# Kernel tuning notes

Measured on AMD Instinct MI355X. Metric: run time of the kernel, lower is better.

Reference implementation:

```python
import jax, jax.numpy as jnp
import numpy as np

D_MODEL = 1024
NUM_HEADS = 16
HEAD_DIM = D_MODEL // NUM_HEADS
LN_EPS = 1e-5


def setup_inputs() -> dict:
    key = jax.random.key(0)
    ks = jax.random.split(key, 10)
    B, S, D = 4, 2048, D_MODEL
    scale = 1.0 / np.sqrt(D)
    inp = {
        'x': jax.random.normal(ks[0], (B, S, D), dtype=jnp.float32),
        'attention_mask': jnp.ones((B, S), dtype=jnp.float32),
        'Wq': jax.random.normal(ks[1], (D, D), dtype=jnp.float32) * scale,
        'bq': jnp.zeros((D,), dtype=jnp.float32),
        'Wk': jax.random.normal(ks[2], (D, D), dtype=jnp.float32) * scale,
        'bk': jnp.zeros((D,), dtype=jnp.float32),
        'Wv': jax.random.normal(ks[3], (D, D), dtype=jnp.float32) * scale,
        'bv': jnp.zeros((D,), dtype=jnp.float32),
        'Wo': jax.random.normal(ks[4], (D, D), dtype=jnp.float32) * scale,
        'bo': jnp.zeros((D,), dtype=jnp.float32),
        'ln_gamma': jnp.ones((D,), dtype=jnp.float32),
        'ln_beta': jnp.zeros((D,), dtype=jnp.float32),
    }
    return inp


def reference(x, attention_mask, Wq, bq, Wk, bk, Wv, bv, Wo, bo, ln_gamma, ln_beta):
    B, S, D = x.shape
    H, Hd = NUM_HEADS, HEAD_DIM
    identity = x
    # LayerNorm (eps matches torch default 1e-5)
    mu = jnp.mean(x, axis=-1, keepdims=True)
    var = jnp.mean(jnp.square(x - mu), axis=-1, keepdims=True)
    xn = (x - mu) / jnp.sqrt(var + LN_EPS) * ln_gamma + ln_beta
    # projections (torch Linear: x @ W.T + b); weights here stored as [out,in]-compatible square
    q = (xn @ Wq.T + bq).reshape(B, S, H, Hd).transpose(0, 2, 1, 3)  # [B,H,S,Hd]
    k = (xn @ Wk.T + bk).reshape(B, S, H, Hd).transpose(0, 2, 1, 3)
    v = (xn @ Wv.T + bv).reshape(B, S, H, Hd).transpose(0, 2, 1, 3)
    scores = jnp.einsum('bhqd,bhkd->bhqk', q, k) / jnp.sqrt(jnp.float32(Hd))
    # padding mask: [B,S] -> additive [B,1,1,S]
    add_mask = (1.0 - attention_mask)[:, None, None, :] * -10000.0
    scores = scores + add_mask
    # causal mask (strict upper triangle -> -inf)
    causal = jnp.triu(jnp.ones((S, S), dtype=bool), k=1)
    scores = jnp.where(causal[None, None, :, :], -jnp.inf, scores)
    attn = jax.nn.softmax(scores, axis=-1)
    out = jnp.einsum('bhqk,bhkd->bhqd', attn, v)  # [B,H,S,Hd]
    out = out.transpose(0, 2, 1, 3).reshape(B, S, D)
    out = out @ Wo.T + bo
    return identity + out
```

## Files before the change

kernel.cpp:

```cpp
#include <hip/hip_runtime.h>

#define D 1024
#define NH 16
#define HD 64
#define SEQ 2048
#define BATCH 4
#define LN_EPS 1e-5f
#define LOG2E 1.44269504088896f

typedef __attribute__((ext_vector_type(8))) __bf16 bf16x8;
typedef __attribute__((ext_vector_type(4))) float f32x4;

__device__ __forceinline__ ushort f2bf(float f) {
    union { float f; uint u; } c; c.f = f;
    uint u = c.u + 0x7fffu + ((c.u >> 16) & 1u);
    return (ushort)(u >> 16);
}

__device__ __forceinline__ void gl_lds16(const ushort* g, ushort* lds) {
    __builtin_amdgcn_global_load_lds(
        (const __attribute__((address_space(1))) void*)g,
        (__attribute__((address_space(3))) void*)lds, 16, 0, 0);
}

__device__ __forceinline__ float exp2_raw(float v) {
    float e;
    asm("v_exp_f32 %0, %1" : "=v"(e) : "v"(v));
    return e;
}

__global__ __launch_bounds__(256) void cvt4(const float* __restrict__ w0,
    const float* __restrict__ w1, const float* __restrict__ w2,
    const float* __restrict__ w3, ushort* __restrict__ out, int n)
{
    int sel = blockIdx.y;
    const float* in = sel == 0 ? w0 : (sel == 1 ? w1 : (sel == 2 ? w2 : w3));
    int i = (blockIdx.x * 256 + threadIdx.x) * 4;
    if (i < n) {
        float4 v = *(const float4*)(in + i);
        ushort4 o;
        o.x = f2bf(v.x); o.y = f2bf(v.y); o.z = f2bf(v.z); o.w = f2bf(v.w);
        *(ushort4*)(out + (size_t)sel * n + i) = o;
    }
}

__global__ __launch_bounds__(256) void ln_kernel(const float* __restrict__ x,
    const float* __restrict__ gamma, const float* __restrict__ beta,
    ushort* __restrict__ xn)
{
    int row = blockIdx.x;
    int tid = threadIdx.x;
    float4 v = ((const float4*)(x + (size_t)row * D))[tid];
    float s = v.x + v.y + v.z + v.w;
#pragma unroll
    for (int off = 32; off > 0; off >>= 1) s += __shfl_down(s, off, 64);
    __shared__ float red1[4], red2[4];
    int wid = tid >> 6, lane = tid & 63;
    if (lane == 0) red1[wid] = s;
    __syncthreads();
    float mean = (red1[0] + red1[1] + red1[2] + red1[3]) * (1.0f / D);
    float dx = v.x - mean, dy = v.y - mean, dz = v.z - mean, dw = v.w - mean;
    float ss = dx * dx + dy * dy + dz * dz + dw * dw;
#pragma unroll
    for (int off = 32; off > 0; off >>= 1) ss += __shfl_down(ss, off, 64);
    if (lane == 0) red2[wid] = ss;
    __syncthreads();
    float var = (red2[0] + red2[1] + red2[2] + red2[3]) * (1.0f / D);
    float rstd = rsqrtf(var + LN_EPS);
    float4 g = ((const float4*)gamma)[tid];
    float4 b = ((const float4*)beta)[tid];
    ushort4 o;
    o.x = f2bf(dx * rstd * g.x + b.x);
    o.y = f2bf(dy * rstd * g.y + b.y);
    o.z = f2bf(dz * rstd * g.z + b.z);
    o.w = f2bf(dw * rstd * g.w + b.w);
    ((ushort4*)(xn + (size_t)row * D))[tid] = o;
}

#define BM 128
#define BKK 64

__global__ __launch_bounds__(256) void gemm_qkv(
    const ushort* __restrict__ A,
    const ushort* __restrict__ W,
    const float* __restrict__ bq, const float* __restrict__ bk,
    const float* __restrict__ bv,
    ushort* __restrict__ Cq, ushort* __restrict__ Ck,
    ushort* __restrict__ CvT,
    int M, int K)
{
    __shared__ ushort As[2][BM * BKK];
    __shared__ ushort Ws[2][BM * BKK];
    const int tid = threadIdx.x;
    const int lane = tid & 63;
    const int wave = tid >> 6;
    const int wr = wave >> 1, wc = wave & 1;
    const int m0 = blockIdx.y * BM;
    const int n0g = blockIdx.x * BM;
    const int region = n0g >> 10;
    const int n0l = n0g & 1023;
    const float* bias = region == 0 ? bq : (region == 1 ? bk : bv);
    const int fr = lane & 15, quad = lane >> 4;
    const int r8 = lane >> 3, c8 = lane & 7;
    const int gc8 = c8 ^ r8;
    const int swf = fr & 7;

    const ushort* gA = A + (size_t)(m0 + wave * 32 + r8) * K + gc8 * 8;
    const ushort* gW = W + (size_t)(n0g + wave * 32 + r8) * K + gc8 * 8;
    const int ldso = (wave * 32) * BKK;

    f32x4 acc[4][4] = {};

#pragma unroll
    for (int t = 0; t < 4; ++t) {
        gl_lds16(gA + (size_t)t * 8 * K, &As[0][ldso + t * 8 * BKK]);
        gl_lds16(gW + (size_t)t * 8 * K, &Ws[0][ldso + t * 8 * BKK]);
    }
    __syncthreads();

    for (int k0 = 0; k0 < K; k0 += BKK) {
        const int cur = (k0 >> 6) & 1;
        if (k0 + BKK < K) {
            const int nxt = cur ^ 1;
#pragma unroll
            for (int t = 0; t < 4; ++t) {
                gl_lds16(gA + (size_t)t * 8 * K + k0 + BKK, &As[nxt][ldso + t * 8 * BKK]);
                gl_lds16(gW + (size_t)t * 8 * K + k0 + BKK, &Ws[nxt][ldso + t * 8 * BKK]);
            }
        }
#pragma unroll
        for (int kh = 0; kh < 2; ++kh) {
            bf16x8 af[4], bf[4];
            const int co = ((kh * 4 + quad) ^ swf) * 8;
#pragma unroll
            for (int i = 0; i < 4; ++i) {
                af[i] = *(const bf16x8*)&As[cur][(wr * 64 + i * 16 + fr) * BKK + co];
                bf[i] = *(const bf16x8*)&Ws[cur][(wc * 64 + i * 16 + fr) * BKK + co];
            }
#pragma unroll
            for (int i = 0; i < 4; ++i)
#pragma unroll
                for (int j = 0; j < 4; ++j)
                    acc[i][j] = __builtin_amdgcn_mfma_f32_16x16x32_bf16(af[i], bf[j], acc[i][j], 0, 0, 0);
        }
        __syncthreads();
    }

#pragma unroll
    for (int j = 0; j < 4; ++j) {
        int col = n0l + wc * 64 + j * 16 + fr;
        float bvl = bias[col];
#pragma unroll
        for (int i = 0; i < 4; ++i) {
#pragma unroll
            for (int r = 0; r < 4; ++r) {
                int row = m0 + wr * 64 + i * 16 + quad * 4 + r;
                ushort hv = f2bf(acc[i][j][r] + bvl);
                if (region == 0) {
                    Cq[(size_t)row * 1024 + col] = hv;
                } else if (region == 1) {
                    Ck[(size_t)row * 1024 + col] = hv;
                } else {
                    int bb = row >> 11, s = row & 2047;
                    int hh = col >> 6, d = col & 63;
                    CvT[(((size_t)bb * NH + hh) * HD + d) * SEQ + s] = hv;
                }
            }
        }
    }
}

__global__ __launch_bounds__(256) void gemm_out(
    const ushort* __restrict__ A, const ushort* __restrict__ W,
    const float* __restrict__ bias, const float* __restrict__ resid,
    float* __restrict__ Cf, int M, int N, int K)
{
    __shared__ ushort As[2][BM * BKK];
    __shared__ ushort Ws[2][BM * BKK];
    const int tid = threadIdx.x;
    const int lane = tid & 63;
    const int wave = tid >> 6;
    const int wr = wave >> 1, wc = wave & 1;
    const int m0 = blockIdx.y * BM, n0 = blockIdx.x * BM;
    const int fr = lane & 15, quad = lane >> 4;
    const int r8 = lane >> 3, c8 = lane & 7;
    const int gc8 = c8 ^ r8;
    const int swf = fr & 7;

    const ushort* gA = A + (size_t)(m0 + wave * 32 + r8) * K + gc8 * 8;
    const ushort* gW = W + (size_t)(n0 + wave * 32 + r8) * K + gc8 * 8;
    const int ldso = (wave * 32) * BKK;

    f32x4 acc[4][4] = {};

#pragma unroll
    for (int t = 0; t < 4; ++t) {
        gl_lds16(gA + (size_t)t * 8 * K, &As[0][ldso + t * 8 * BKK]);
        gl_lds16(gW + (size_t)t * 8 * K, &Ws[0][ldso + t * 8 * BKK]);
    }
    __syncthreads();

    for (int k0 = 0; k0 < K; k0 += BKK) {
        const int cur = (k0 >> 6) & 1;
        if (k0 + BKK < K) {
            const int nxt = cur ^ 1;
#pragma unroll
            for (int t = 0; t < 4; ++t) {
                gl_lds16(gA + (size_t)t * 8 * K + k0 + BKK, &As[nxt][ldso + t * 8 * BKK]);
                gl_lds16(gW + (size_t)t * 8 * K + k0 + BKK, &Ws[nxt][ldso + t * 8 * BKK]);
            }
        }
#pragma unroll
        for (int kh = 0; kh < 2; ++kh) {
            bf16x8 af[4], bf[4];
            const int co = ((kh * 4 + quad) ^ swf) * 8;
#pragma unroll
            for (int i = 0; i < 4; ++i) {
                af[i] = *(const bf16x8*)&As[cur][(wr * 64 + i * 16 + fr) * BKK + co];
                bf[i] = *(const bf16x8*)&Ws[cur][(wc * 64 + i * 16 + fr) * BKK + co];
            }
#pragma unroll
            for (int i = 0; i < 4; ++i)
#pragma unroll
                for (int j = 0; j < 4; ++j)
                    acc[i][j] = __builtin_amdgcn_mfma_f32_16x16x32_bf16(af[i], bf[j], acc[i][j], 0, 0, 0);
        }
        __syncthreads();
    }

#pragma unroll
    for (int j = 0; j < 4; ++j) {
        int col = n0 + wc * 64 + j * 16 + fr;
        float bvl = bias[col];
#pragma unroll
        for (int i = 0; i < 4; ++i) {
#pragma unroll
            for (int r = 0; r < 4; ++r) {
                int row = m0 + wr * 64 + i * 16 + quad * 4 + r;
                Cf[(size_t)row * N + col] =
                    acc[i][j][r] + bvl + resid[(size_t)row * N + col];
            }
        }
    }
}

#define PSP 72
__global__ __launch_bounds__(256, 3) void flash_mfma(
    const ushort* __restrict__ Q, const ushort* __restrict__ K,
    const ushort* __restrict__ VtG, const float* __restrict__ mask,
    ushort* __restrict__ O)
{
    const int id = blockIdx.x;
    const int bx = id >> 6;
    const int hb = id & 63;
    const int h = hb & 15, b = hb >> 4;
    __shared__ ushort Ks[2][64 * 64];
    __shared__ ushort Vt[2][64 * 64];
    __shared__ ushort Ps[128 * PSP];
    const int tid = threadIdx.x;
    const int lane = tid & 63, wave = tid >> 6;
    const int fr = lane & 15, quad = lane >> 4;
    const int srow = tid >> 3;
    const int sc8 = tid & 7;
    const int g8 = sc8 ^ (srow & 7);
    const int swf = fr & 7;

    const ushort* gK0 = K + (size_t)(b * SEQ) * D + h * HD + (size_t)srow * D + g8 * 8;
    const ushort* gK1 = gK0 + (size_t)32 * D;
    const ushort* gV0 = VtG + ((size_t)(b * NH + h) * HD + srow) * SEQ + g8 * 8;
    const ushort* gV1 = gV0 + (size_t)32 * SEQ;
    const float* mrow = mask + (size_t)b * SEQ;
    const float SCALE2 = 0.125f * LOG2E;
    const float MASKC = -10000.0f * LOG2E;

    for (int phase = 0; phase < 2; ++phase) {
        const int qt = phase ? (15 - bx) : bx;
        const int q0 = qt * 128;
        bf16x8 qf[2][2];
#pragma unroll
        for (int s = 0; s < 2; ++s) {
            const ushort* qptr = Q + ((size_t)(b * SEQ + q0 + s * 64 + wave * 16 + fr)) * D
                                   + h * HD + quad * 8;
            qf[s][0] = *(const bf16x8*)(qptr);
            qf[s][1] = *(const bf16x8*)(qptr + 32);
        }

        f32x4 oacc[2][4] = {};
        float lsum[2][4] = {};
        const int nkb = 2 * qt + 2;

        gl_lds16(gK0, &Ks[0][wave * 512]);
        gl_lds16(gK1, &Ks[0][2048 + wave * 512]);
        gl_lds16(gV0, &Vt[0][wave * 512]);
        gl_lds16(gV1, &Vt[0][2048 + wave * 512]);
        __syncthreads();

        for (int kb = 0; kb < nkb; ++kb) {
            const int cur = kb & 1;
            if (kb + 1 < nkb) {
                const int nxt = cur ^ 1;
                gl_lds16(gK0 + (size_t)(kb + 1) * 64 * D, &Ks[nxt][wave * 512]);
                gl_lds16(gK1 + (size_t)(kb + 1) * 64 * D, &Ks[nxt][2048 + wave * 512]);
                gl_lds16(gV0 + (kb + 1) * 64, &Vt[nxt][wave * 512]);
                gl_lds16(gV1 + (kb + 1) * 64, &Vt[nxt][2048 + wave * 512]);
            }
            f32x4 mv[4];
#pragma unroll
            for (int jt = 0; jt < 4; ++jt)
                mv[jt] = ((const f32x4*)(mrow + kb * 64))[jt * 4 + quad];

            const bool s0act = (kb <= 2 * qt);

            f32x4 sacc[2][4] = {};
            __builtin_amdgcn_s_setprio(1);
#pragma unroll
            for (int jt = 0; jt < 4; ++jt) {
                const int rb = (jt * 16 + fr) * 64;
                bf16x8 kf0 = *(const bf16x8*)&Ks[cur][rb + ((quad) ^ swf) * 8];
                bf16x8 kf1 = *(const bf16x8*)&Ks[cur][rb + ((4 + quad) ^ swf) * 8];
                sacc[0][jt] = __builtin_amdgcn_mfma_f32_16x16x32_bf16(kf0, qf[0][0], sacc[0][jt], 0, 0, 0);
                sacc[0][jt] = __builtin_amdgcn_mfma_f32_16x16x32_bf16(kf1, qf[0][1], sacc[0][jt], 0, 0, 0);
                sacc[1][jt] = __builtin_amdgcn_mfma_f32_16x16x32_bf16(kf0, qf[1][0], sacc[1][jt], 0, 0, 0);
                sacc[1][jt] = __builtin_amdgcn_mfma_f32_16x16x32_bf16(kf1, qf[1][1], sacc[1][jt], 0, 0, 0);
            }
            __builtin_amdgcn_s_setprio(0);

            float padd[4][4];
#pragma unroll
            for (int jt = 0; jt < 4; ++jt)
#pragma unroll
                for (int r = 0; r < 4; ++r)
                    padd[jt][r] = fmaf(mv[jt][r], -MASKC, MASKC);
            const int ql = wave * 16 + fr;
#pragma unroll
            for (int s = 0; s < 2; ++s) {
                if (s == 0 && !s0act) continue;
                const bool diag = (kb == 2 * qt + s);
#pragma unroll
                for (int jt = 0; jt < 4; ++jt) {
                    float p[4];
#pragma unroll
                    for (int r = 0; r < 4; ++r) {
                        float v = fmaf(sacc[s][jt][r], SCALE2, padd[jt][r]);
                        if (diag) {
                            int keyl = jt * 16 + quad * 4 + r;
                            v = (keyl > ql) ? -1e30f : v;
                        }
                        float e = exp2_raw(v);
                        p[r] = e;
                        lsum[s][r] += e;
                    }
                    uint w0, w1;
                    asm("v_cvt_pk_bf16_f32 %0, %1, %2" : "=v"(w0) : "v"(p[0]), "v"(p[1]));
                    asm("v_cvt_pk_bf16_f32 %0, %1, %2" : "=v"(w1) : "v"(p[2]), "v"(p[3]));
                    union { uint2 u; ushort4 us; } pu;
                    pu.u.x = w0; pu.u.y = w1;
                    *(ushort4*)&Ps[(s * 64 + wave * 16 + fr) * PSP + jt * 16 + quad * 4] = pu.us;
                }
            }

            bf16x8 pa[2][2];
#pragma unroll
            for (int s = 0; s < 2; ++s) {
                pa[s][0] = *(const bf16x8*)&Ps[(s * 64 + wave * 16 + fr) * PSP + quad * 8];
                pa[s][1] = *(const bf16x8*)&Ps[(s * 64 + wave * 16 + fr) * PSP + 32 + quad * 8];
            }
            __builtin_amdgcn_s_setprio(1);
#pragma unroll
            for (int dt = 0; dt < 4; ++dt) {
                const int rb = (dt * 16 + fr) * 64;
                bf16x8 vf0 = *(const bf16x8*)&Vt[cur][rb + ((quad) ^ swf) * 8];
                bf16x8 vf1 = *(const bf16x8*)&Vt[cur][rb + ((4 + quad) ^ swf) * 8];
                if (s0act) {
                    oacc[0][dt] = __builtin_amdgcn_mfma_f32_16x16x32_bf16(pa[0][0], vf0, oacc[0][dt], 0, 0, 0);
                    oacc[0][dt] = __builtin_amdgcn_mfma_f32_16x16x32_bf16(pa[0][1], vf1, oacc[0][dt], 0, 0, 0);
                }
                oacc[1][dt] = __builtin_amdgcn_mfma_f32_16x16x32_bf16(pa[1][0], vf0, oacc[1][dt], 0, 0, 0);
                oacc[1][dt] = __builtin_amdgcn_mfma_f32_16x16x32_bf16(pa[1][1], vf1, oacc[1][dt], 0, 0, 0);
            }
            __builtin_amdgcn_s_setprio(0);
            __syncthreads();
        }

#pragma unroll
        for (int s = 0; s < 2; ++s) {
            float lt = (lsum[s][0] + lsum[s][1]) + (lsum[s][2] + lsum[s][3]);
            lt += __shfl_xor(lt, 16, 64);
            lt += __shfl_xor(lt, 32, 64);
            float linv[4];
#pragma unroll
            for (int r = 0; r < 4; ++r)
                linv[r] = 1.0f / __shfl(lt, quad * 4 + r, 64);
#pragma unroll
            for (int dt = 0; dt < 4; ++dt)
#pragma unroll
                for (int r = 0; r < 4; ++r) {
                    int q = q0 + s * 64 + wave * 16 + quad * 4 + r;
                    O[((size_t)(b * SEQ + q)) * D + h * HD + dt * 16 + fr] =
                        f2bf(oacc[s][dt][r] * linv[r]);
                }
        }
    }
}

extern "C" void kernel_launch(void* const* d_in, const int* in_sizes, int n_in,
                              void* d_out, int out_size, void* d_ws, size_t ws_size,
                              hipStream_t stream)
{
    const float* x     = (const float*)d_in[0];
    const float* amask = (const float*)d_in[1];
    const float* Wq    = (const float*)d_in[2];
    const float* bq    = (const float*)d_in[3];
    const float* Wk    = (const float*)d_in[4];
    const float* bk    = (const float*)d_in[5];
    const float* Wv    = (const float*)d_in[6];
    const float* bv    = (const float*)d_in[7];
    const float* Wo    = (const float*)d_in[8];
    const float* bo    = (const float*)d_in[9];
    const float* gamma = (const float*)d_in[10];
    const float* beta  = (const float*)d_in[11];
    float* out = (float*)d_out;

    const size_t MROWS = (size_t)BATCH * SEQ;
    const size_t MB = 1024 * 1024;
    char* ws = (char*)d_ws;
    ushort* Qb    = (ushort*)(ws);
    ushort* Kb    = (ushort*)(ws + 16 * MB);
    ushort* Vtb   = (ushort*)(ws + 32 * MB);
    ushort* xn_bf = (ushort*)(ws + 48 * MB);
    ushort* Wq_bf = (ushort*)(ws + 64 * MB);
    ushort* Wo_bf = (ushort*)(ws + 70 * MB);
    ushort* attn_bf = xn_bf;

    const int WN = D * D;
    cvt4<<<dim3(WN / 1024, 4), 256, 0, stream>>>(Wq, Wk, Wv, Wo, Wq_bf, WN);

    ln_kernel<<<dim3((unsigned)MROWS), 256, 0, stream>>>(x, gamma, beta, xn_bf);

    gemm_qkv<<<dim3(24, 64), 256, 0, stream>>>(xn_bf, Wq_bf, bq, bk, bv,
                                               Qb, Kb, Vtb, (int)MROWS, D);

    flash_mfma<<<dim3(512), 256, 0, stream>>>(Qb, Kb, Vtb, amask, attn_bf);

    gemm_out<<<dim3(8, 64), 256, 0, stream>>>(attn_bf, Wo_bf, bo, x, out,
                                              (int)MROWS, D, D);
}
```

Baseline: 282.8 us.

## Enlarge QKV GEMM tile to 256x256 with 8 waves and manual waitcnt pipelining

The QKV projection GEMM moves from 128x128 tiles with 4 waves to 256x256 tiles with 8 waves. Each wave now computes a 128x64 sub-tile, which raises arithmetic intensity per LDS load. The __syncthreads pairs are replaced with explicit s_waitcnt vmcnt/lgkmcnt plus s_barrier, so the next tile's global-to-LDS loads can overlap compute. The cost is 128KB of LDS, higher register pressure from 32 accumulators, and fewer blocks (384) to fill the CUs.

After: 297.6 us. 1.05x slower.

```diff
diff --git a/kernel.cpp b/kernel.cpp
--- a/kernel.cpp
+++ b/kernel.cpp
@@ -80,7 +80,7 @@
 #define BM 128
 #define BKK 64
 
-__global__ __launch_bounds__(256) void gemm_qkv(
+__global__ __launch_bounds__(512, 2) void gemm_qkv(
     const ushort* __restrict__ A,
     const ushort* __restrict__ W,
     const float* __restrict__ bq, const float* __restrict__ bk,
@@ -89,14 +89,14 @@
     ushort* __restrict__ CvT,
     int M, int K)
 {
-    __shared__ ushort As[2][BM * BKK];
-    __shared__ ushort Ws[2][BM * BKK];
+    __shared__ ushort As[2][256 * BKK];
+    __shared__ ushort Ws[2][256 * BKK];
     const int tid = threadIdx.x;
     const int lane = tid & 63;
     const int wave = tid >> 6;
-    const int wr = wave >> 1, wc = wave & 1;
-    const int m0 = blockIdx.y * BM;
-    const int n0g = blockIdx.x * BM;
+    const int wm = wave >> 2, wn = wave & 3;
+    const int m0 = blockIdx.y * 256;
+    const int n0g = blockIdx.x * 256;
     const int region = n0g >> 10;
     const int n0l = n0g & 1023;
     const float* bias = region == 0 ? bq : (region == 1 ? bk : bv);
@@ -109,52 +109,60 @@
     const ushort* gW = W + (size_t)(n0g + wave * 32 + r8) * K + gc8 * 8;
     const int ldso = (wave * 32) * BKK;
 
-    f32x4 acc[4][4] = {};
+    f32x4 acc[8][4] = {};
 
 #pragma unroll
     for (int t = 0; t < 4; ++t) {
         gl_lds16(gA + (size_t)t * 8 * K, &As[0][ldso + t * 8 * BKK]);
         gl_lds16(gW + (size_t)t * 8 * K, &Ws[0][ldso + t * 8 * BKK]);
     }
-    __syncthreads();
-
-    for (int k0 = 0; k0 < K; k0 += BKK) {
-        const int cur = (k0 >> 6) & 1;
-        if (k0 + BKK < K) {
-            const int nxt = cur ^ 1;
+
+    const int NT = K / BKK;
+    for (int kt = 0; kt < NT; ++kt) {
+        const int c = kt & 1;
+        if (kt + 1 < NT) {
+            const int nx = c ^ 1;
+            const int k1 = (kt + 1) * BKK;
 #pragma unroll
             for (int t = 0; t < 4; ++t) {
-                gl_lds16(gA + (size_t)t * 8 * K + k0 + BKK, &As[nxt][ldso + t * 8 * BKK]);
-                gl_lds16(gW + (size_t)t * 8 * K + k0 + BKK, &Ws[nxt][ldso + t * 8 * BKK]);
-            }
-        }
+                gl_lds16(gA + (size_t)t * 8 * K + k1, &As[nx][ldso + t * 8 * BKK]);
+                gl_lds16(gW + (size_t)t * 8 * K + k1, &Ws[nx][ldso + t * 8 * BKK]);
+            }
+            asm volatile("s_waitcnt vmcnt(8)" ::: "memory");
+        } else {
+            asm volatile("s_waitcnt vmcnt(0)" ::: "memory");
+        }
+        __builtin_amdgcn_s_barrier();
+        __builtin_amdgcn_sched_barrier(0);
 #pragma unroll
         for (int kh = 0; kh < 2; ++kh) {
-            bf16x8 af[4], bf[4];
+            bf16x8 af[8], bf[4];
             const int co = ((kh * 4 + quad) ^ swf) * 8;
 #pragma unroll
-            for (int i = 0; i < 4; ++i) {
-                af[i] = *(const bf16x8*)&As[cur][(wr * 64 + i * 16 + fr) * BKK + co];
-                bf[i] = *(const bf16x8*)&Ws[cur][(wc * 64 + i * 16 + fr) * BKK + co];
-            }
-#pragma unroll
-            for (int i = 0; i < 4; ++i)
+            for (int i = 0; i < 8; ++i)
+                af[i] = *(const bf16x8*)&As[c][(wm * 128 + i * 16 + fr) * BKK + co];
+#pragma unroll
+            for (int j = 0; j < 4; ++j)
+                bf[j] = *(const bf16x8*)&Ws[c][(wn * 64 + j * 16 + fr) * BKK + co];
+#pragma unroll
+            for (int i = 0; i < 8; ++i)
 #pragma unroll
                 for (int j = 0; j < 4; ++j)
                     acc[i][j] = __builtin_amdgcn_mfma_f32_16x16x32_bf16(af[i], bf[j], acc[i][j], 0, 0, 0);
         }
-        __syncthreads();
+        asm volatile("s_waitcnt lgkmcnt(0)" ::: "memory");
+        __builtin_amdgcn_s_barrier();
     }
 
 #pragma unroll
     for (int j = 0; j < 4; ++j) {
-        int col = n0l + wc * 64 + j * 16 + fr;
+        int col = n0l + wn * 64 + j * 16 + fr;
         float bvl = bias[col];
 #pragma unroll
-        for (int i = 0; i < 4; ++i) {
+        for (int i = 0; i < 8; ++i) {
 #pragma unroll
             for (int r = 0; r < 4; ++r) {
-                int row = m0 + wr * 64 + i * 16 + quad * 4 + r;
+                int row = m0 + wm * 128 + i * 16 + quad * 4 + r;
                 ushort hv = f2bf(acc[i][j][r] + bvl);
                 if (region == 0) {
                     Cq[(size_t)row * 1024 + col] = hv;
@@ -437,7 +445,7 @@
 
     ln_kernel<<<dim3((unsigned)MROWS), 256, 0, stream>>>(x, gamma, beta, xn_bf);
 
-    gemm_qkv<<<dim3(24, 64), 256, 0, stream>>>(xn_bf, Wq_bf, bq, bk, bv,
+    gemm_qkv<<<dim3(12, 32), 512, 0, stream>>>(xn_bf, Wq_bf, bq, bk, bv,
                                                Qb, Kb, Vtb, (int)MROWS, D);
 
     flash_mfma<<<dim3(512), 256, 0, stream>>>(Qb, Kb, Vtb, amask, attn_bf);
```
